# Performance work log

Measured on AMD Instinct MI355X. Metric: run time of the kernel, lower is better.

The kernel has to match this reference:

```python
import jax, jax.numpy as jnp
import numpy as np

N_NODES = 100000
NUM_REL = 2


def rgcn_conv(x, src, dst, etype, W, root, bias):
    """PyG-style RGCNConv: per-relation mean aggregation + root transform + bias.
    x: [N, in], W: [R, in, out], root: [in, out], bias: [out].
    """
    R = W.shape[0]
    N = x.shape[0]
    # Pre-transform nodes by every relation weight: [R, N, out]
    xr = jnp.einsum('ni,rio->rno', x, W)
    msgs = xr[etype, src]  # [E, out] gather per-edge, relation-typed
    seg_id = dst * R + etype  # combined (node, relation) segment id
    summed = jax.ops.segment_sum(msgs, seg_id, num_segments=N * R)
    cnt = jax.ops.segment_sum(jnp.ones(etype.shape, x.dtype), seg_id, num_segments=N * R)
    summed = summed.reshape(N, R, -1)
    cnt = cnt.reshape(N, R, 1)
    agg = (summed / jnp.maximum(cnt, 1.0)).sum(axis=1)  # sum over relations of per-relation means
    return agg + x @ root + bias


def setup_inputs() -> dict:
    key = jax.random.key(0)
    ks = jax.random.split(key, 9)
    d = 128
    E = 800000
    sc = 1.0 / np.sqrt(d)
    return {
        'x': jax.random.normal(ks[0], (N_NODES, d), jnp.float32),
        'edge_index_a': jax.random.randint(ks[1], (2, E), 0, N_NODES, jnp.int64),
        'edge_index_b': jax.random.randint(ks[2], (2, E), 0, N_NODES, jnp.int64),
        'W1': jax.random.normal(ks[3], (NUM_REL, d, d), jnp.float32) * sc,
        'root1': jax.random.normal(ks[4], (d, d), jnp.float32) * sc,
        'b1': jnp.zeros((d,), jnp.float32),
        'W2': jax.random.normal(ks[5], (NUM_REL, d, d), jnp.float32) * sc,
        'root2': jax.random.normal(ks[6], (d, d), jnp.float32) * sc,
        'b2': jnp.zeros((d,), jnp.float32),
    }


def reference(x, edge_index_a, edge_index_b, W1, root1, b1, W2, root2, b2):
    # Concatenate per-relation edge lists + build edge_type ids (a->0, b->1)
    edge_index = jnp.concatenate([edge_index_a, edge_index_b], axis=1)
    etype = jnp.concatenate([
        jnp.zeros((edge_index_a.shape[1],), jnp.int32),
        jnp.ones((edge_index_b.shape[1],), jnp.int32),
    ])
    src, dst = edge_index[0], edge_index[1]
    h = rgcn_conv(x, src, dst, etype, W1, root1, b1)
    h = jax.nn.relu(h)
    out = rgcn_conv(h, src, dst, etype, W2, root2, b2)
    return out
```

## Files before the change

kernel.cpp:

```cpp
#include <hip/hip_runtime.h>
#include <hip/hip_bf16.h>


typedef __attribute__((ext_vector_type(8))) short bf16x8;
typedef __attribute__((ext_vector_type(4))) float f32x4;
typedef unsigned short ushort_t;
typedef unsigned int uint_t;

#define BSHIFT 9
#define SEGB (1 << (BSHIFT + 1))
#define NBMAX 256
#define CH_PER_THREAD 16
#define CHUNK (256 * CH_PER_THREAD)

#define GBM 256
#define KCH 128
#define LDBE 136

__device__ __forceinline__ float b2fu(uint_t u) {
  union { uint_t u; float f; } v;
  v.u = u << 16;
  return v.f;
}
__device__ __forceinline__ ushort_t f2b(float f) {
  union { float f; uint_t u; } v;
  v.f = f;
  uint_t u = v.u;
  return (ushort_t)((u + 0x7FFFu + ((u >> 16) & 1u)) >> 16);
}

__global__ __launch_bounds__(256) void prep(
    const float* __restrict__ W1, const float* __restrict__ root1,
    const float* __restrict__ W2, const float* __restrict__ root2,
    ushort_t* __restrict__ Bt1, ushort_t* __restrict__ Bt2,
    const float* __restrict__ x, ushort_t* __restrict__ aggbuf1, int N,
    const int* __restrict__ ea, const int* __restrict__ eb, int E, int NB,
    int* __restrict__ bucket_cnt, int XSB) {
  __shared__ int h[NBMAX];
  int b = blockIdx.x;
  if (b < 384) {
    int flat = b * 256 + threadIdx.x;
    int which = flat >= 49152;
    int idx = flat - which * 49152;
    int c = idx / 384;
    int k = idx - c * 384;
    const float* W = which ? W2 : W1;
    const float* root = which ? root2 : root1;
    ushort_t* Bt = which ? Bt2 : Bt1;
    float v = (k < 256) ? W[(size_t)k * 128 + c] : root[(size_t)(k - 256) * 128 + c];
    Bt[(size_t)c * 384 + k] = f2b(v);
  } else if (b < 384 + XSB) {
    int idx = (b - 384) * 256 + threadIdx.x;
    int n = idx >> 6, lane = idx & 63;
    if (n < N) {
      float2 v = *(const float2*)(x + (size_t)n * 128 + lane * 2);
      uint_t pk = (uint_t)f2b(v.x) | ((uint_t)f2b(v.y) << 16);
      *(uint_t*)(aggbuf1 + (size_t)n * 384 + 256 + lane * 2) = pk;
    }
  } else {
    for (int i = threadIdx.x; i < NB; i += 256) h[i] = 0;
    __syncthreads();
    int tbase = (b - 384 - XSB) * CHUNK + threadIdx.x;
    int total = 2 * E;
#pragma unroll
    for (int j = 0; j < CH_PER_THREAD; ++j) {
      int i = tbase + j * 256;
      if (i < total) {
        int dst = (i < E) ? ea[E + i] : eb[i];
        atomicAdd(&h[dst >> BSHIFT], 1);
      }
    }
    __syncthreads();
    for (int i = threadIdx.x; i < NB; i += 256)
      if (h[i]) atomicAdd(&bucket_cnt[i], h[i]);
  }
}

__global__ __launch_bounds__(256) void bucket_bin(
    const int* __restrict__ ea, const int* __restrict__ eb,
    int E, int NB, const int* __restrict__ bucket_cnt,
    int* __restrict__ bucket_cursor, uint2* __restrict__ staging) {
  __shared__ int h[NBMAX];
  __shared__ int bbase[NBMAX];
  __shared__ int gbase[NBMAX];
  __shared__ int sdata[256];
  int t = threadIdx.x;
  int v = (t < NB) ? bucket_cnt[t] : 0;
  sdata[t] = v;
  __syncthreads();
  for (int off = 1; off < 256; off <<= 1) {
    int tmp = (t >= off) ? sdata[t - off] : 0;
    __syncthreads();
    sdata[t] += tmp;
    __syncthreads();
  }
  if (t < NB) gbase[t] = sdata[t] - v;
  for (int i = t; i < NB; i += 256) h[i] = 0;
  __syncthreads();

  int tbase = blockIdx.x * CHUNK + t;
  int total = 2 * E;
  uint2 val[CH_PER_THREAD];
#pragma unroll
  for (int j = 0; j < CH_PER_THREAD; ++j) {
    int i = tbase + j * 256;
    if (i < total) {
      int src, dst, rel;
      if (i < E) { src = ea[i];     dst = ea[E + i]; rel = 0; }
      else       { src = eb[i - E]; dst = eb[i];     rel = 1; }
      val[j].x = (uint_t)src;
      val[j].y = (uint_t)(dst * 2 + rel);
      atomicAdd(&h[dst >> BSHIFT], 1);
    } else {
      val[j].y = 0xffffffffu;
    }
  }
  __syncthreads();
  for (int i = t; i < NB; i += 256) {
    int c = h[i];
    bbase[i] = c ? gbase[i] + atomicAdd(&bucket_cursor[i], c) : 0;
    h[i] = 0;
  }
  __syncthreads();
#pragma unroll
  for (int j = 0; j < CH_PER_THREAD; ++j) {
    if (val[j].y != 0xffffffffu) {
      int bkt = (int)(val[j].y >> (BSHIFT + 1));
      int r = atomicAdd(&h[bkt], 1);
      staging[(size_t)bbase[bkt] + r] = val[j];
    }
  }
}

__global__ __launch_bounds__(256) void bucket_build(
    const uint2* __restrict__ staging, const int* __restrict__ bucket_cnt,
    int NB, int* __restrict__ csr, int* __restrict__ offs,
    int* __restrict__ ends, int nseg) {
  __shared__ int scnt[SEGB];
  __shared__ int sexcl[SEGB];
  __shared__ int sdata[256];
  int b = blockIdx.x;
  int t = threadIdx.x;
  int v = (t < NB) ? bucket_cnt[t] : 0;
  sdata[t] = v;
  __syncthreads();
  for (int off = 1; off < 256; off <<= 1) {
    int tmp = (t >= off) ? sdata[t - off] : 0;
    __syncthreads();
    sdata[t] += tmp;
    __syncthreads();
  }
  int base = sdata[b] - bucket_cnt[b];
  int ne = bucket_cnt[b];
  int seg0 = b << (BSHIFT + 1);
  __syncthreads();

  for (int i = t; i < SEGB; i += 256) scnt[i] = 0;
  __syncthreads();
  const uint2* st = staging + base;
  for (int i = t; i < ne; i += 256) {
    int seg = (int)st[i].y - seg0;
    atomicAdd(&scnt[seg], 1);
  }
  __syncthreads();
  int c0 = scnt[t * 4 + 0], c1 = scnt[t * 4 + 1];
  int c2 = scnt[t * 4 + 2], c3 = scnt[t * 4 + 3];
  int s = c0 + c1 + c2 + c3;
  sdata[t] = s;
  __syncthreads();
  for (int off = 1; off < 256; off <<= 1) {
    int tmp = (t >= off) ? sdata[t - off] : 0;
    __syncthreads();
    sdata[t] += tmp;
    __syncthreads();
  }
  int excl = sdata[t] - s;
  int e0 = excl, e1 = excl + c0, e2 = e1 + c1, e3 = e2 + c2;
  sexcl[t * 4 + 0] = e0;
  sexcl[t * 4 + 1] = e1;
  sexcl[t * 4 + 2] = e2;
  sexcl[t * 4 + 3] = e3;
  {
    int g = seg0 + t * 4;
    if (g + 0 < nseg) { offs[g + 0] = base + e0; ends[g + 0] = base + e0 + c0; }
    if (g + 1 < nseg) { offs[g + 1] = base + e1; ends[g + 1] = base + e1 + c1; }
    if (g + 2 < nseg) { offs[g + 2] = base + e2; ends[g + 2] = base + e2 + c2; }
    if (g + 3 < nseg) { offs[g + 3] = base + e3; ends[g + 3] = base + e3 + c3; }
  }
  scnt[t * 4 + 0] = 0;
  scnt[t * 4 + 1] = 0;
  scnt[t * 4 + 2] = 0;
  scnt[t * 4 + 3] = 0;
  __syncthreads();
  for (int i = t; i < ne; i += 256) {
    uint2 vrec = st[i];
    int seg = (int)vrec.y - seg0;
    int r = atomicAdd(&scnt[seg], 1);
    csr[base + sexcl[seg] + r] = (int)vrec.x;
  }
}

__device__ __forceinline__ void accum8(float* acc, uint4 v) {
  acc[0] += b2fu(v.x); acc[1] += b2fu(v.x >> 16);
  acc[2] += b2fu(v.y); acc[3] += b2fu(v.y >> 16);
  acc[4] += b2fu(v.z); acc[5] += b2fu(v.z >> 16);
  acc[6] += b2fu(v.w); acc[7] += b2fu(v.w >> 16);
}

__global__ __launch_bounds__(256) void agg_kernel(
    const ushort_t* __restrict__ xb,
    const int* __restrict__ csr,
    const int* __restrict__ offs, const int* __restrict__ ends,
    ushort_t* __restrict__ agg, int nseg) {
  int wid = (blockIdx.x * blockDim.x + threadIdx.x) >> 6;
  if (wid >= nseg) return;
  int lane = threadIdx.x & 63;
  int q = lane >> 4;
  int t = lane & 15;
  int beg = offs[wid], end = ends[wid];

  float acc[8];
#pragma unroll
  for (int j = 0; j < 8; ++j) acc[j] = 0.f;

  int e = beg + q;
  for (; e + 4 < end; e += 8) {
    int s0 = csr[e];
    int s1 = csr[e + 4];
    uint4 v0 = *(const uint4*)(xb + (size_t)s0 * 384 + 256 + t * 8);
    uint4 v1 = *(const uint4*)(xb + (size_t)s1 * 384 + 256 + t * 8);
    accum8(acc, v0);
    accum8(acc, v1);
  }
  if (e < end) {
    int s0 = csr[e];
    uint4 v0 = *(const uint4*)(xb + (size_t)s0 * 384 + 256 + t * 8);
    accum8(acc, v0);
  }

#pragma unroll
  for (int j = 0; j < 8; ++j) {
    acc[j] += __shfl_xor(acc[j], 16);
    acc[j] += __shfl_xor(acc[j], 32);
  }

  int c = end - beg;
  float inv = 1.0f / (float)(c > 1 ? c : 1);
  if (q == 0) {
    uint4 o;
    o.x = (uint_t)f2b(acc[0] * inv) | ((uint_t)f2b(acc[1] * inv) << 16);
    o.y = (uint_t)f2b(acc[2] * inv) | ((uint_t)f2b(acc[3] * inv) << 16);
    o.z = (uint_t)f2b(acc[4] * inv) | ((uint_t)f2b(acc[5] * inv) << 16);
    o.w = (uint_t)f2b(acc[6] * inv) | ((uint_t)f2b(acc[7] * inv) << 16);
    int n = wid >> 1, r = wid & 1;
    *(uint4*)(agg + (size_t)n * 384 + r * 128 + t * 8) = o;
  }
}


__device__ __forceinline__ void do_mfma32(
    const char* bs, f32x4 (&acc)[4][8], const bf16x8 (&a)[4],
    int ks, int lrow, int kg) {
  bf16x8 b[8];
#pragma unroll
  for (int c = 0; c < 8; ++c)
    b[c] = *(const bf16x8*)(bs + (c * 16 + lrow) * (LDBE * 2) +
                            (ks * 4 + kg) * 16);
#pragma unroll
  for (int r = 0; r < 4; ++r)
#pragma unroll
    for (int c = 0; c < 8; ++c)
      acc[r][c] = __builtin_amdgcn_mfma_f32_16x16x32_bf16(a[r], b[c], acc[r][c], 0, 0, 0);
}

template <int MODE>
__global__ __launch_bounds__(256, 2) void mfma_gemm(
    const ushort_t* __restrict__ A,
    const ushort_t* __restrict__ Bt,
    const float* __restrict__ bias,
    float* __restrict__ outf,
    ushort_t* __restrict__ outb,
    int M) {
  __shared__ __align__(16) ushort_t Bs[2][128 * LDBE];
  const int tid = threadIdx.x;
  const int lane = tid & 63;
  const int wave = tid >> 6;
  const int lrow = lane & 15;
  const int kg = lane >> 4;
  const int rowbase = blockIdx.x * GBM + wave * 64;

  f32x4 acc[4][8];
#pragma unroll
  for (int r = 0; r < 4; ++r)
#pragma unroll
    for (int c = 0; c < 8; ++c) acc[r][c] = (f32x4){0.f, 0.f, 0.f, 0.f};

  uint4 stg[8];
#pragma unroll
  for (int j = 0; j < 8; ++j) {
    int flat = tid + j * 256;
    int col = flat >> 4;
    int q = flat & 15;
    stg[j] = *(const uint4*)(Bt + (size_t)col * 384 + q * 8);
  }
#pragma unroll
  for (int j = 0; j < 8; ++j) {
    int flat = tid + j * 256;
    int col = flat >> 4;
    int q = flat & 15;
    *(uint4*)((char*)&Bs[0][0] + col * (LDBE * 2) + q * 16) = stg[j];
  }
  __syncthreads();

  int cur = 0;
  for (int ch = 0; ch < 3; ++ch) {
    if (ch < 2) {
#pragma unroll
      for (int j = 0; j < 8; ++j) {
        int flat = tid + j * 256;
        int col = flat >> 4;
        int q = flat & 15;
        stg[j] = *(const uint4*)(Bt + (size_t)col * 384 + (ch + 1) * KCH + q * 8);
      }
    }
    const ushort_t* ab = A + (size_t)ch * KCH + kg * 8;
    const char* bsbase = (const char*)&Bs[0][0] + cur * (128 * LDBE * 2);
    bf16x8 aA[4], aB[4];
#pragma unroll
    for (int r = 0; r < 4; ++r)
      aA[r] = *(const bf16x8*)(ab + (size_t)(rowbase + r * 16 + lrow) * 384);
#pragma unroll
    for (int r = 0; r < 4; ++r)
      aB[r] = *(const bf16x8*)(ab + (size_t)(rowbase + r * 16 + lrow) * 384 + 32);
    do_mfma32(bsbase, acc, aA, 0, lrow, kg);
#pragma unroll
    for (int r = 0; r < 4; ++r)
      aA[r] = *(const bf16x8*)(ab + (size_t)(rowbase + r * 16 + lrow) * 384 + 64);
    do_mfma32(bsbase, acc, aB, 1, lrow, kg);
#pragma unroll
    for (int r = 0; r < 4; ++r)
      aB[r] = *(const bf16x8*)(ab + (size_t)(rowbase + r * 16 + lrow) * 384 + 96);
    do_mfma32(bsbase, acc, aA, 2, lrow, kg);
    do_mfma32(bsbase, acc, aB, 3, lrow, kg);
    if (ch < 2) {
#pragma unroll
      for (int j = 0; j < 8; ++j) {
        int flat = tid + j * 256;
        int col = flat >> 4;
        int q = flat & 15;
        *(uint4*)((char*)&Bs[0][0] + (cur ^ 1) * (128 * LDBE * 2) +
                  col * (LDBE * 2) + q * 16) = stg[j];
      }
      __syncthreads();
      cur ^= 1;
    }
  }

#pragma unroll
  for (int c = 0; c < 8; ++c) {
    int col = c * 16 + lrow;
    float bv = bias[col];
#pragma unroll
    for (int r = 0; r < 4; ++r) {
      int r0 = rowbase + r * 16 + kg * 4;
#pragma unroll
      for (int j = 0; j < 4; ++j) {
        int row = r0 + j;
        if (row < M) {
          float v = acc[r][c][j] + bv;
          if (MODE == 1) {
            v = fmaxf(v, 0.f);
            outb[(size_t)row * 384 + 256 + col] = f2b(v);
          } else {
            outf[(size_t)row * 128 + col] = v;
          }
        }
      }
    }
  }
}

extern "C" void kernel_launch(void* const* d_in, const int* in_sizes, int n_in,
                              void* d_out, int out_size, void* d_ws, size_t ws_size,
                              hipStream_t stream) {
  const float* x     = (const float*)d_in[0];
  const int*   ea    = (const int*)d_in[1];
  const int*   eb    = (const int*)d_in[2];
  const float* W1    = (const float*)d_in[3];
  const float* root1 = (const float*)d_in[4];
  const float* b1    = (const float*)d_in[5];
  const float* W2    = (const float*)d_in[6];
  const float* root2 = (const float*)d_in[7];
  const float* b2    = (const float*)d_in[8];
  float* out = (float*)d_out;

  const int N = in_sizes[0] / 128;
  const int E = in_sizes[1] / 2;
  const int nseg = N * 2;
  const int Mblk = (N + GBM - 1) / GBM;
  const int Mpad = Mblk * GBM;
  const int NB = ((N - 1) >> BSHIFT) + 1;
  const int nchunk = (2 * E + CHUNK - 1) / CHUNK;
  const int XSB = (N * 64 + 255) / 256;

  char* p = (char*)d_ws;
  ushort_t* aggbuf1 = (ushort_t*)p;  p += (size_t)Mpad * 384 * sizeof(ushort_t);
  ushort_t* aggbuf2 = (ushort_t*)p;  p += (size_t)Mpad * 384 * sizeof(ushort_t);
  ushort_t* Bt1 = (ushort_t*)p;      p += (size_t)128 * 384 * sizeof(ushort_t);
  ushort_t* Bt2 = (ushort_t*)p;      p += (size_t)128 * 384 * sizeof(ushort_t);
  int* csr = (int*)p;                p += (size_t)2 * E * sizeof(int);
  int* offs = (int*)p;               p += (size_t)nseg * sizeof(int);
  int* ends = (int*)p;               p += (size_t)nseg * sizeof(int);
  int* bucket_cnt = (int*)p;         p += NBMAX * sizeof(int);
  int* bucket_cursor = (int*)p;      p += NBMAX * sizeof(int);
  uint2* staging = (uint2*)aggbuf2;

  hipMemsetAsync(bucket_cnt, 0, 2 * NBMAX * sizeof(int), stream);

  prep<<<384 + XSB + nchunk, 256, 0, stream>>>(
      W1, root1, W2, root2, Bt1, Bt2, x, aggbuf1, N,
      ea, eb, E, NB, bucket_cnt, XSB);

  bucket_bin<<<nchunk, 256, 0, stream>>>(ea, eb, E, NB, bucket_cnt,
                                         bucket_cursor, staging);
  bucket_build<<<NB, 256, 0, stream>>>(staging, bucket_cnt, NB,
                                       csr, offs, ends, nseg);

  const int agg_blocks = (nseg + 3) / 4;

  agg_kernel<<<agg_blocks, 256, 0, stream>>>(aggbuf1, csr, offs, ends, aggbuf1, nseg);
  mfma_gemm<1><<<Mblk, 256, 0, stream>>>(aggbuf1, Bt1, b1, nullptr, aggbuf2, N);

  agg_kernel<<<agg_blocks, 256, 0, stream>>>(aggbuf2, csr, offs, ends, aggbuf2, nseg);
  mfma_gemm<0><<<Mblk, 256, 0, stream>>>(aggbuf2, Bt2, b2, out, nullptr, N);
}
```

Baseline: 342.4 us.

## Pack staging records into 32 bits, store byte offsets in CSR, use dot2 accumulation

Staging records shrink from uint2 to one packed uint (source index shifted left by 10, local segment id in the low bits), halving staging traffic in the bin and build kernels. The CSR now holds precomputed byte offsets (src*768+512) rather than node indices, which drops the address arithmetic from the aggregation loop. The bf16-to-fp32 unpack-and-add is replaced with v_dot2_f32_bf16 against a 1.0 selector, so each element costs one instruction. The risks are overflow in the packing and in the int byte offset for large N, and the dot2 path's rounding behaviour.

Result: no change. 347.7 us (+1.5%).

```diff
diff --git a/kernel.cpp b/kernel.cpp
--- a/kernel.cpp
+++ b/kernel.cpp
@@ -17,6 +17,9 @@
 #define KCH 128
 #define LDBE 136
 
+#define ROWB 768
+#define XOFF 512
+
 __device__ __forceinline__ float b2fu(uint_t u) {
   union { uint_t u; float f; } v;
   v.u = u << 16;
@@ -27,6 +30,9 @@
   v.f = f;
   uint_t u = v.u;
   return (ushort_t)((u + 0x7FFFu + ((u >> 16) & 1u)) >> 16);
+}
+__device__ __forceinline__ void dot2acc(float& a, uint_t pk, uint_t sel) {
+  asm("v_dot2_f32_bf16 %0, %1, %2, %0" : "+v"(a) : "v"(pk), "v"(sel));
 }
 
 __global__ __launch_bounds__(256) void prep(
@@ -79,7 +85,7 @@
 __global__ __launch_bounds__(256) void bucket_bin(
     const int* __restrict__ ea, const int* __restrict__ eb,
     int E, int NB, const int* __restrict__ bucket_cnt,
-    int* __restrict__ bucket_cursor, uint2* __restrict__ staging) {
+    int* __restrict__ bucket_cursor, uint_t* __restrict__ staging) {
   __shared__ int h[NBMAX];
   __shared__ int bbase[NBMAX];
   __shared__ int gbase[NBMAX];
@@ -100,7 +106,8 @@
 
   int tbase = blockIdx.x * CHUNK + t;
   int total = 2 * E;
-  uint2 val[CH_PER_THREAD];
+  uint_t val[CH_PER_THREAD];
+  short bktv[CH_PER_THREAD];
 #pragma unroll
   for (int j = 0; j < CH_PER_THREAD; ++j) {
     int i = tbase + j * 256;
@@ -108,11 +115,13 @@
       int src, dst, rel;
       if (i < E) { src = ea[i];     dst = ea[E + i]; rel = 0; }
       else       { src = eb[i - E]; dst = eb[i];     rel = 1; }
-      val[j].x = (uint_t)src;
-      val[j].y = (uint_t)(dst * 2 + rel);
-      atomicAdd(&h[dst >> BSHIFT], 1);
+      int seg = dst * 2 + rel;
+      int bkt = seg >> (BSHIFT + 1);
+      val[j] = ((uint_t)src << 10) | (uint_t)(seg & (SEGB - 1));
+      bktv[j] = (short)bkt;
+      atomicAdd(&h[bkt], 1);
     } else {
-      val[j].y = 0xffffffffu;
+      bktv[j] = -1;
     }
   }
   __syncthreads();
@@ -124,8 +133,8 @@
   __syncthreads();
 #pragma unroll
   for (int j = 0; j < CH_PER_THREAD; ++j) {
-    if (val[j].y != 0xffffffffu) {
-      int bkt = (int)(val[j].y >> (BSHIFT + 1));
+    if (bktv[j] >= 0) {
+      int bkt = bktv[j];
       int r = atomicAdd(&h[bkt], 1);
       staging[(size_t)bbase[bkt] + r] = val[j];
     }
@@ -133,7 +142,7 @@
 }
 
 __global__ __launch_bounds__(256) void bucket_build(
-    const uint2* __restrict__ staging, const int* __restrict__ bucket_cnt,
+    const uint_t* __restrict__ staging, const int* __restrict__ bucket_cnt,
     int NB, int* __restrict__ csr, int* __restrict__ offs,
     int* __restrict__ ends, int nseg) {
   __shared__ int scnt[SEGB];
@@ -157,10 +166,9 @@
 
   for (int i = t; i < SEGB; i += 256) scnt[i] = 0;
   __syncthreads();
-  const uint2* st = staging + base;
+  const uint_t* st = staging + base;
   for (int i = t; i < ne; i += 256) {
-    int seg = (int)st[i].y - seg0;
-    atomicAdd(&scnt[seg], 1);
+    atomicAdd(&scnt[st[i] & (SEGB - 1)], 1);
   }
   __syncthreads();
   int c0 = scnt[t * 4 + 0], c1 = scnt[t * 4 + 1];
@@ -193,22 +201,16 @@
   scnt[t * 4 + 3] = 0;
   __syncthreads();
   for (int i = t; i < ne; i += 256) {
-    uint2 vrec = st[i];
-    int seg = (int)vrec.y - seg0;
+    uint_t rec = st[i];
+    int seg = (int)(rec & (SEGB - 1));
+    int src = (int)(rec >> 10);
     int r = atomicAdd(&scnt[seg], 1);
-    csr[base + sexcl[seg] + r] = (int)vrec.x;
-  }
-}
-
-__device__ __forceinline__ void accum8(float* acc, uint4 v) {
-  acc[0] += b2fu(v.x); acc[1] += b2fu(v.x >> 16);
-  acc[2] += b2fu(v.y); acc[3] += b2fu(v.y >> 16);
-  acc[4] += b2fu(v.z); acc[5] += b2fu(v.z >> 16);
-  acc[6] += b2fu(v.w); acc[7] += b2fu(v.w >> 16);
+    csr[base + sexcl[seg] + r] = src * ROWB + XOFF;
+  }
 }
 
 __global__ __launch_bounds__(256) void agg_kernel(
-    const ushort_t* __restrict__ xb,
+    const char* __restrict__ xbc,
     const int* __restrict__ csr,
     const int* __restrict__ offs, const int* __restrict__ ends,
     ushort_t* __restrict__ agg, int nseg) {
@@ -218,24 +220,36 @@
   int q = lane >> 4;
   int t = lane & 15;
   int beg = offs[wid], end = ends[wid];
+  const uint_t sel_lo = 0x00003F80u;
+  const uint_t sel_hi = 0x3F800000u;
 
   float acc[8];
 #pragma unroll
   for (int j = 0; j < 8; ++j) acc[j] = 0.f;
 
+  const char* xt = xbc + t * 16;
   int e = beg + q;
   for (; e + 4 < end; e += 8) {
-    int s0 = csr[e];
-    int s1 = csr[e + 4];
-    uint4 v0 = *(const uint4*)(xb + (size_t)s0 * 384 + 256 + t * 8);
-    uint4 v1 = *(const uint4*)(xb + (size_t)s1 * 384 + 256 + t * 8);
-    accum8(acc, v0);
-    accum8(acc, v1);
+    int o0 = csr[e];
+    int o1 = csr[e + 4];
+    uint4 v0 = *(const uint4*)(xt + o0);
+    uint4 v1 = *(const uint4*)(xt + o1);
+    dot2acc(acc[0], v0.x, sel_lo); dot2acc(acc[1], v0.x, sel_hi);
+    dot2acc(acc[2], v0.y, sel_lo); dot2acc(acc[3], v0.y, sel_hi);
+    dot2acc(acc[4], v0.z, sel_lo); dot2acc(acc[5], v0.z, sel_hi);
+    dot2acc(acc[6], v0.w, sel_lo); dot2acc(acc[7], v0.w, sel_hi);
+    dot2acc(acc[0], v1.x, sel_lo); dot2acc(acc[1], v1.x, sel_hi);
+    dot2acc(acc[2], v1.y, sel_lo); dot2acc(acc[3], v1.y, sel_hi);
+    dot2acc(acc[4], v1.z, sel_lo); dot2acc(acc[5], v1.z, sel_hi);
+    dot2acc(acc[6], v1.w, sel_lo); dot2acc(acc[7], v1.w, sel_hi);
   }
   if (e < end) {
-    int s0 = csr[e];
-    uint4 v0 = *(const uint4*)(xb + (size_t)s0 * 384 + 256 + t * 8);
-    accum8(acc, v0);
+    int o0 = csr[e];
+    uint4 v0 = *(const uint4*)(xt + o0);
+    dot2acc(acc[0], v0.x, sel_lo); dot2acc(acc[1], v0.x, sel_hi);
+    dot2acc(acc[2], v0.y, sel_lo); dot2acc(acc[3], v0.y, sel_hi);
+    dot2acc(acc[4], v0.z, sel_lo); dot2acc(acc[5], v0.z, sel_hi);
+    dot2acc(acc[6], v0.w, sel_lo); dot2acc(acc[7], v0.w, sel_hi);
   }
 
 #pragma unroll
@@ -256,7 +270,6 @@
     *(uint4*)(agg + (size_t)n * 384 + r * 128 + t * 8) = o;
   }
 }
-
 
 __device__ __forceinline__ void do_mfma32(
     const char* bs, f32x4 (&acc)[4][8], const bf16x8 (&a)[4],
@@ -413,7 +426,7 @@
   int* ends = (int*)p;               p += (size_t)nseg * sizeof(int);
   int* bucket_cnt = (int*)p;         p += NBMAX * sizeof(int);
   int* bucket_cursor = (int*)p;      p += NBMAX * sizeof(int);
-  uint2* staging = (uint2*)aggbuf2;
+  uint_t* staging = (uint_t*)aggbuf2;
 
   hipMemsetAsync(bucket_cnt, 0, 2 * NBMAX * sizeof(int), stream);
 
@@ -428,9 +441,11 @@
 
   const int agg_blocks = (nseg + 3) / 4;
 
-  agg_kernel<<<agg_blocks, 256, 0, stream>>>(aggbuf1, csr, offs, ends, aggbuf1, nseg);
+  agg_kernel<<<agg_blocks, 256, 0, stream>>>((const char*)aggbuf1, csr, offs,
+                                             ends, aggbuf1, nseg);
   mfma_gemm<1><<<Mblk, 256, 0, stream>>>(aggbuf1, Bt1, b1, nullptr, aggbuf2, N);
 
-  agg_kernel<<<agg_blocks, 256, 0, stream>>>(aggbuf2, csr, offs, ends, aggbuf2, nseg);
+  agg_kernel<<<agg_blocks, 256, 0, stream>>>((const char*)aggbuf2, csr, offs,
+                                             ends, aggbuf2, nseg);
   mfma_gemm<0><<<Mblk, 256, 0, stream>>>(aggbuf2, Bt2, b2, out, nullptr, N);
 }
```
